# Kernel tuning notes

Hardware: AMD Instinct MI355X
Metric: run time of the kernel (lower is better)

The kernel has to match this reference:

```python
import jax, jax.numpy as jnp
import numpy as np

B, OBS, TASK = 65536, 512, 128
D, M, N = 64, 32, 4  # embedding dim, module width, modules per layer


def setup_inputs() -> dict:
    key = jax.random.key(0)
    ks = jax.random.split(key, 16)

    def w(k, shape):
        fan_in = shape[-2]
        return jax.random.normal(k, shape, jnp.float32) * np.float32(np.sqrt(2.0 / fan_in))

    z = lambda *s: jnp.zeros(s, jnp.float32)
    return dict(
        obs=jax.random.normal(ks[0], (B, OBS), jnp.float32),
        task=jax.random.normal(ks[1], (B, TASK), jnp.float32),
        Ws1=w(ks[2], (OBS, D)), bs1=z(D),
        Ws2=w(ks[3], (D, D)), bs2=z(D),
        Wt=w(ks[4], (TASK, D)), bt=z(D),
        Wa0=w(ks[5], (D, N * N)), ba0=z(N * N),
        Wa1=w(ks[6], (D, N * N)), ba1=z(N * N),
        Wc0=w(ks[7], (N * N, D)), bc0=z(D),
        Wc1=w(ks[8], (2 * N * N, D)), bc1=z(D),
        We0=w(ks[9], (N, D, M)), be0=z(N, M),
        We1=w(ks[10], (N, M, M)), be1=z(N, M),
        We2=w(ks[11], (N, M, M)), be2=z(N, M),
    )


def reference(obs, task, Ws1, bs1, Ws2, bs2, Wt, bt, Wa0, ba0, Wa1, ba1,
              Wc0, bc0, Wc1, bc1, We0, be0, We1, be1, We2, be2):
    relu = jax.nn.relu
    # base encoders
    s = relu(relu(obs @ Ws1 + bs1) @ Ws2 + bs2)          # [B, D]
    t = relu(task @ Wt + bt)                              # [B, D]
    r0 = s * t                                            # first routing inputs [B, D]
    prev = jnp.broadcast_to(s[None], (N,) + s.shape)      # [N, B, D] (state emb fed to all layer-0 modules)

    # routing layer 0 -> 1
    a0 = jax.nn.softmax((r0 @ Wa0 + ba0).reshape(-1, N, N), axis=-1)   # [B, N_next, N_prev]
    m = relu(jnp.einsum('nbi,nio->nbo', prev, We0) + be0[:, None, :])  # [N, B, M] expert outputs
    prev = jnp.einsum('bij,jbd->ibd', a0, m)                           # [N, B, M] attention-combined
    r = relu((a0.reshape(-1, N * N) @ Wc0 + bc0) * r0)                 # updated routing inputs

    # routing layer 1 -> 2
    a1 = jax.nn.softmax((r @ Wa1 + ba1).reshape(-1, N, N), axis=-1)
    m = relu(jnp.einsum('nbi,nio->nbo', prev, We1) + be1[:, None, :])
    prev = jnp.einsum('bij,jbd->ibd', a1, m)
    attn_cat = jnp.concatenate([a0.reshape(-1, N * N), a1.reshape(-1, N * N)], axis=-1)
    r = relu((attn_cat @ Wc1 + bc1) * r0)  # computed as in original (unused afterward)

    # final module layer, plain sum over modules
    m = relu(jnp.einsum('nbi,nio->nbo', prev, We2) + be2[:, None, :])  # [N, B, M]
    return relu(m.sum(axis=0))                                          # [B, M]
```

## Files before the change

### kernel.cpp

```cpp
#include <hip/hip_runtime.h>
#include <hip/hip_bf16.h>


using f32x4 = __attribute__((ext_vector_type(4))) float;
using h16x4 = __attribute__((ext_vector_type(4))) _Float16;

#define MFMA16(a, b, c) __builtin_amdgcn_mfma_f32_16x16x16f16((a), (b), (c), 0, 0, 0)

__device__ __forceinline__ short h_bits(float f) {
  _Float16 h = (_Float16)f;
  return __builtin_bit_cast(short, h);
}

__device__ __forceinline__ void dma16(const void* g, void* l) {
  __builtin_amdgcn_global_load_lds(
      (const __attribute__((address_space(1))) unsigned int*)g,
      (__attribute__((address_space(3))) unsigned int*)l, 16, 0, 0);
}

__global__ void sm_convert_v4(
    const float* __restrict__ Ws1, const float* __restrict__ Ws2, const float* __restrict__ Wt,
    const float* __restrict__ Wa0, const float* __restrict__ Wa1, const float* __restrict__ Wc0,
    const float* __restrict__ We0, const float* __restrict__ We1, const float* __restrict__ We2,
    const float* __restrict__ bs1, const float* __restrict__ bs2, const float* __restrict__ bt,
    const float* __restrict__ ba0, const float* __restrict__ ba1, const float* __restrict__ bc0,
    const float* __restrict__ be0, const float* __restrict__ be1, const float* __restrict__ be2,
    short* __restrict__ wsh, float* __restrict__ biasf) {
  int d = blockIdx.x * 256 + threadIdx.x;
  if (d < 64512) {
    float v;
    if (d < 32768) {
      int kk = d & 3, nt = (d >> 2) & 3, p = (d >> 4) & 15, q = (d >> 8) & 3, c = d >> 10;
      int k = c * 16 + q * 4 + kk, o = nt * 16 + p;
      v = Ws1[k * 64 + o];
    }
    else if (d < 36864) { int r = d - 32768, o = r >> 6, k = r & 63;   v = Ws2[k * 64 + o]; }
    else if (d < 45056) {
      int r = d - 36864;
      int kk = r & 3, nt = (r >> 2) & 3, p = (r >> 4) & 15, q = (r >> 8) & 3, c = r >> 10;
      int k = c * 16 + q * 4 + kk, o = nt * 16 + p;
      v = Wt[k * 64 + o];
    }
    else if (d < 46080) { int r = d - 45056, o = r >> 6, k = r & 63;   v = Wa0[k * 16 + o]; }
    else if (d < 47104) { int r = d - 46080, o = r >> 6, k = r & 63;   v = Wa1[k * 16 + o]; }
    else if (d < 48128) { int r = d - 47104, o = r >> 4, k = r & 15;   v = Wc0[k * 64 + o]; }
    else if (d < 56320) { int r = d - 48128, n = r >> 11, o = (r >> 6) & 31, i = r & 63; v = We0[n * 2048 + i * 32 + o]; }
    else if (d < 60416) { int r = d - 56320, n = r >> 10, o = (r >> 5) & 31, i = r & 31; v = We1[n * 1024 + i * 32 + o]; }
    else                { int r = d - 60416, n = r >> 10, o = (r >> 5) & 31, i = r & 31; v = We2[n * 1024 + i * 32 + o]; }
    wsh[d] = h_bits(v);
  } else if (d < 65184) {
    int r = d - 64512;
    float v;
    if      (r < 64)  v = bs1[r];
    else if (r < 128) v = bs2[r - 64];
    else if (r < 192) v = bt[r - 128];
    else if (r < 208) v = ba0[r - 192];
    else if (r < 224) v = ba1[r - 208];
    else if (r < 288) v = bc0[r - 224];
    else if (r < 416) v = be0[r - 288];
    else if (r < 544) v = be1[r - 416];
    else              v = be2[r - 544];
    biasf[r] = v;
  }
}

__global__ __launch_bounds__(256) void sm_fused_v4(
    const float* __restrict__ obs, const float* __restrict__ task,
    const short* __restrict__ wsh, const float* __restrict__ biasf,
    float* __restrict__ out) {
  const int tid  = threadIdx.x;
  const int wave = tid >> 6;
  const int lane = tid & 63;
  const int q    = lane >> 4;
  const int p    = lane & 15;
  const int lrow = wave * 16;
  const int rowblk = blockIdx.x * 64 + lrow;

  __shared__ __align__(16) char lds[9216 + 3072 + 8192 + 20480];
  char* x_lds = lds;
  char* a_lds = lds + 9216;
  char* ring  = lds + 12288 + wave * 2048;
  char* p_lds = lds + 20480;

  const short* Bp1  = wsh;
  const short* Ws2T = wsh + 32768;
  const short* WtP  = wsh + 36864;
  const short* Wa0T = wsh + 45056;
  const short* Wa1T = wsh + 46080;
  const short* Wc0T = wsh + 47104;
  const short* We0T = wsh + 48128;
  const short* We1T = wsh + 56320;
  const short* We2T = wsh + 60416;
  const float* bs1 = biasf;        const float* bs2 = biasf + 64;
  const float* bt  = biasf + 128;  const float* ba0 = biasf + 192;
  const float* ba1 = biasf + 208;  const float* bc0 = biasf + 224;
  const float* be0 = biasf + 288;  const float* be1 = biasf + 416;
  const float* be2 = biasf + 544;

  const f32x4 z4 = {0.f, 0.f, 0.f, 0.f};

  auto stx  = [&](int row, int col, float v) { *(short*)(x_lds + row * 144 + col * 2) = h_bits(v); };
  auto ldx4 = [&](int row, int k0) -> h16x4 { return *(const h16x4*)(x_lds + row * 144 + k0 * 2); };
  auto ldb  = [&](const short* W, int off) -> h16x4 { return *(const h16x4*)(W + off); };
  auto cvt4 = [&](const float4& v) -> h16x4 {
    h16x4 a;
    a[0] = (_Float16)v.x; a[1] = (_Float16)v.y;
    a[2] = (_Float16)v.z; a[3] = (_Float16)v.w;
    return a;
  };

  f32x4 accX[4] = {z4, z4, z4, z4};
  {
    const float* srow = obs + (size_t)(rowblk + (lane >> 2)) * 512 + (lane & 3) * 4;
    dma16(srow, ring);
    for (int c = 0; c < 32; ++c) {
      if (c + 1 < 32) {
        dma16(srow + (c + 1) * 16, ring + ((c + 1) & 1) * 1024);
        asm volatile("s_waitcnt vmcnt(1)" ::: "memory");
      } else {
        asm volatile("s_waitcnt vmcnt(0)" ::: "memory");
      }
      const char* sb = ring + (c & 1) * 1024;
      h16x4 a = cvt4(*(const float4*)(sb + p * 64 + q * 16));
      const short* bp = Bp1 + ((c * 4 + q) * 16 + p) * 16;
#pragma unroll
      for (int nt = 0; nt < 4; ++nt)
        accX[nt] = MFMA16(a, ldb(bp, nt * 4), accX[nt]);
    }
  }
#pragma unroll
  for (int nt = 0; nt < 4; ++nt) {
    float bias = bs1[nt * 16 + p];
#pragma unroll
    for (int r = 0; r < 4; ++r)
      stx(lrow + 4 * q + r, nt * 16 + p, fmaxf(accX[nt][r] + bias, 0.f));
  }

  f32x4 accS[4] = {z4, z4, z4, z4};
#pragma unroll
  for (int kb = 0; kb < 4; ++kb) {
    h16x4 a = ldx4(lrow + p, kb * 16 + q * 4);
#pragma unroll
    for (int nt = 0; nt < 4; ++nt)
      accS[nt] = MFMA16(a, ldb(Ws2T, (nt * 16 + p) * 64 + kb * 16 + q * 4), accS[nt]);
  }
  float sf[4][4];
#pragma unroll
  for (int nt = 0; nt < 4; ++nt) {
    float bias = bs2[nt * 16 + p];
#pragma unroll
    for (int r = 0; r < 4; ++r) sf[nt][r] = fmaxf(accS[nt][r] + bias, 0.f);
  }
#pragma unroll
  for (int nt = 0; nt < 4; ++nt)
#pragma unroll
    for (int r = 0; r < 4; ++r) stx(lrow + 4 * q + r, nt * 16 + p, sf[nt][r]);

  f32x4 accT[4] = {z4, z4, z4, z4};
  {
    const float* srow = task + (size_t)(rowblk + (lane >> 2)) * 128 + (lane & 3) * 4;
    dma16(srow, ring);
    for (int c = 0; c < 8; ++c) {
      if (c + 1 < 8) {
        dma16(srow + (c + 1) * 16, ring + ((c + 1) & 1) * 1024);
        asm volatile("s_waitcnt vmcnt(1)" ::: "memory");
      } else {
        asm volatile("s_waitcnt vmcnt(0)" ::: "memory");
      }
      const char* sb = ring + (c & 1) * 1024;
      h16x4 a = cvt4(*(const float4*)(sb + p * 64 + q * 16));
      const short* bp = WtP + ((c * 4 + q) * 16 + p) * 16;
#pragma unroll
      for (int nt = 0; nt < 4; ++nt)
        accT[nt] = MFMA16(a, ldb(bp, nt * 4), accT[nt]);
    }
  }
  float r0f[4][4];
#pragma unroll
  for (int nt = 0; nt < 4; ++nt) {
    float bias = bt[nt * 16 + p];
#pragma unroll
    for (int r = 0; r < 4; ++r)
      r0f[nt][r] = sf[nt][r] * fmaxf(accT[nt][r] + bias, 0.f);
  }

  float mfr[4][2][4];
#pragma unroll
  for (int n = 0; n < 4; ++n) {
    f32x4 acc[2] = {z4, z4};
#pragma unroll
    for (int kb = 0; kb < 4; ++kb) {
      h16x4 a = ldx4(lrow + p, kb * 16 + q * 4);
#pragma unroll
      for (int nt = 0; nt < 2; ++nt)
        acc[nt] = MFMA16(a, ldb(We0T, (n * 32 + nt * 16 + p) * 64 + kb * 16 + q * 4), acc[nt]);
    }
#pragma unroll
    for (int nt = 0; nt < 2; ++nt) {
      float bias = be0[n * 32 + nt * 16 + p];
#pragma unroll
      for (int r = 0; r < 4; ++r) mfr[n][nt][r] = fmaxf(acc[nt][r] + bias, 0.f);
    }
  }

#pragma unroll
  for (int nt = 0; nt < 4; ++nt)
#pragma unroll
    for (int r = 0; r < 4; ++r) stx(lrow + 4 * q + r, nt * 16 + p, r0f[nt][r]);

  f32x4 accA = z4;
#pragma unroll
  for (int kb = 0; kb < 4; ++kb)
    accA = MFMA16(ldx4(lrow + p, kb * 16 + q * 4), ldb(Wa0T, p * 64 + kb * 16 + q * 4), accA);
  float a0v[4];
  {
    float bias = ba0[p];
#pragma unroll
    for (int r = 0; r < 4; ++r) {
      float v = accA[r] + bias;
      float mx = fmaxf(v, __shfl_xor(v, 1));
      mx = fmaxf(mx, __shfl_xor(mx, 2));
      float e = __expf(v - mx);
      float ssum = e + __shfl_xor(e, 1);
      ssum += __shfl_xor(ssum, 2);
      a0v[r] = e / ssum;
    }
  }
#pragma unroll
  for (int r = 0; r < 4; ++r)
    *(short*)(a_lds + (lrow + 4 * q + r) * 48 + p * 2) = h_bits(a0v[r]);

  float pv[4][2][4];
#pragma unroll
  for (int i = 0; i < 4; ++i)
#pragma unroll
    for (int nt = 0; nt < 2; ++nt)
#pragma unroll
      for (int r = 0; r < 4; ++r) pv[i][nt][r] = 0.f;
  const int sbase = lane & 48;
#pragma unroll
  for (int r = 0; r < 4; ++r) {
#pragma unroll
    for (int c = 0; c < 16; ++c) {
      float av = __shfl(a0v[r], sbase | c);
      pv[c >> 2][0][r] += av * mfr[c & 3][0][r];
      pv[c >> 2][1][r] += av * mfr[c & 3][1][r];
    }
  }

  f32x4 accC[4] = {z4, z4, z4, z4};
  {
    h16x4 a = *(const h16x4*)(a_lds + (lrow + p) * 48 + q * 8);
#pragma unroll
    for (int nt = 0; nt < 4; ++nt)
      accC[nt] = MFMA16(a, ldb(Wc0T, (nt * 16 + p) * 16 + q * 4), accC[nt]);
  }
  float rf[4][4];
#pragma unroll
  for (int nt = 0; nt < 4; ++nt) {
    float bias = bc0[nt * 16 + p];
#pragma unroll
    for (int r = 0; r < 4; ++r)
      rf[nt][r] = fmaxf((accC[nt][r] + bias) * r0f[nt][r], 0.f);
  }
#pragma unroll
  for (int nt = 0; nt < 4; ++nt)
#pragma unroll
    for (int r = 0; r < 4; ++r) stx(lrow + 4 * q + r, nt * 16 + p, rf[nt][r]);

  f32x4 accA1 = z4;
#pragma unroll
  for (int kb = 0; kb < 4; ++kb)
    accA1 = MFMA16(ldx4(lrow + p, kb * 16 + q * 4), ldb(Wa1T, p * 64 + kb * 16 + q * 4), accA1);
  float a1v[4];
  {
    float bias = ba1[p];
#pragma unroll
    for (int r = 0; r < 4; ++r) {
      float v = accA1[r] + bias;
      float mx = fmaxf(v, __shfl_xor(v, 1));
      mx = fmaxf(mx, __shfl_xor(mx, 2));
      float e = __expf(v - mx);
      float ssum = e + __shfl_xor(e, 1);
      ssum += __shfl_xor(ssum, 2);
      a1v[r] = e / ssum;
    }
  }

#pragma unroll
  for (int i = 0; i < 4; ++i)
#pragma unroll
    for (int nt = 0; nt < 2; ++nt)
#pragma unroll
      for (int r = 0; r < 4; ++r)
        *(short*)(p_lds + (i * 64 + lrow + 4 * q + r) * 80 + (nt * 16 + p) * 2) = h_bits(pv[i][nt][r]);

  float m1f[4][2][4];
#pragma unroll
  for (int n = 0; n < 4; ++n) {
    f32x4 acc[2] = {z4, z4};
#pragma unroll
    for (int kb = 0; kb < 2; ++kb) {
      h16x4 a = *(const h16x4*)(p_lds + (n * 64 + lrow + p) * 80 + kb * 32 + q * 8);
#pragma unroll
      for (int nt = 0; nt < 2; ++nt)
        acc[nt] = MFMA16(a, ldb(We1T, (n * 32 + nt * 16 + p) * 32 + kb * 16 + q * 4), acc[nt]);
    }
#pragma unroll
    for (int nt = 0; nt < 2; ++nt) {
      float bias = be1[n * 32 + nt * 16 + p];
#pragma unroll
      for (int r = 0; r < 4; ++r) m1f[n][nt][r] = fmaxf(acc[nt][r] + bias, 0.f);
    }
  }

#pragma unroll
  for (int i = 0; i < 4; ++i)
#pragma unroll
    for (int nt = 0; nt < 2; ++nt)
#pragma unroll
      for (int r = 0; r < 4; ++r) pv[i][nt][r] = 0.f;
#pragma unroll
  for (int r = 0; r < 4; ++r) {
#pragma unroll
    for (int c = 0; c < 16; ++c) {
      float av = __shfl(a1v[r], sbase | c);
      pv[c >> 2][0][r] += av * m1f[c & 3][0][r];
      pv[c >> 2][1][r] += av * m1f[c & 3][1][r];
    }
  }

#pragma unroll
  for (int i = 0; i < 4; ++i)
#pragma unroll
    for (int nt = 0; nt < 2; ++nt)
#pragma unroll
      for (int r = 0; r < 4; ++r)
        *(short*)(p_lds + (i * 64 + lrow + 4 * q + r) * 80 + (nt * 16 + p) * 2) = h_bits(pv[i][nt][r]);

  float of[2][4] = {{0.f, 0.f, 0.f, 0.f}, {0.f, 0.f, 0.f, 0.f}};
#pragma unroll
  for (int n = 0; n < 4; ++n) {
    f32x4 acc[2] = {z4, z4};
#pragma unroll
    for (int kb = 0; kb < 2; ++kb) {
      h16x4 a = *(const h16x4*)(p_lds + (n * 64 + lrow + p) * 80 + kb * 32 + q * 8);
#pragma unroll
      for (int nt = 0; nt < 2; ++nt)
        acc[nt] = MFMA16(a, ldb(We2T, (n * 32 + nt * 16 + p) * 32 + kb * 16 + q * 4), acc[nt]);
    }
#pragma unroll
    for (int nt = 0; nt < 2; ++nt) {
      float bias = be2[n * 32 + nt * 16 + p];
#pragma unroll
      for (int r = 0; r < 4; ++r) of[nt][r] += fmaxf(acc[nt][r] + bias, 0.f);
    }
  }
#pragma unroll
  for (int nt = 0; nt < 2; ++nt)
#pragma unroll
    for (int r = 0; r < 4; ++r) {
      int grow = rowblk + 4 * q + r;
      out[(size_t)grow * 32 + nt * 16 + p] = of[nt][r];
    }
}

extern "C" void kernel_launch(void* const* d_in, const int* in_sizes, int n_in,
                              void* d_out, int out_size, void* d_ws, size_t ws_size,
                              hipStream_t stream) {
  (void)in_sizes; (void)n_in; (void)out_size; (void)ws_size;
  const float* obs  = (const float*)d_in[0];
  const float* task = (const float*)d_in[1];
  const float* Ws1 = (const float*)d_in[2];  const float* bs1 = (const float*)d_in[3];
  const float* Ws2 = (const float*)d_in[4];  const float* bs2 = (const float*)d_in[5];
  const float* Wt  = (const float*)d_in[6];  const float* bt  = (const float*)d_in[7];
  const float* Wa0 = (const float*)d_in[8];  const float* ba0 = (const float*)d_in[9];
  const float* Wa1 = (const float*)d_in[10]; const float* ba1 = (const float*)d_in[11];
  const float* Wc0 = (const float*)d_in[12]; const float* bc0 = (const float*)d_in[13];
  const float* We0 = (const float*)d_in[16]; const float* be0 = (const float*)d_in[17];
  const float* We1 = (const float*)d_in[18]; const float* be1 = (const float*)d_in[19];
  const float* We2 = (const float*)d_in[20]; const float* be2 = (const float*)d_in[21];

  short* wsh   = (short*)d_ws;
  float* biasf = (float*)((char*)d_ws + 129040);

  sm_convert_v4<<<dim3(255), dim3(256), 0, stream>>>(
      Ws1, Ws2, Wt, Wa0, Wa1, Wc0, We0, We1, We2,
      bs1, bs2, bt, ba0, ba1, bc0, be0, be1, be2,
      wsh, biasf);
  sm_fused_v4<<<dim3(1024), dim3(256), 0, stream>>>(
      obs, task, wsh, biasf, (float*)d_out);
}
```

Baseline: 82.62 us.

## Replace LDS DMA ring with register-prefetched direct loads and alias LDS buffers

The obs and task GEMM input streams no longer go through a global_load_lds double-buffered ring. They now load directly into registers with a three-deep prefetch, fetching A fragments and B weight fragments as 16-byte vectors. The per-chunk waitcnt stalls and the LDS round trip are dropped. The p_lds buffer is aliased onto the x_lds/a_lds region behind a new __syncthreads, cutting LDS from about 40KB to 20KB so more blocks can be resident. The cost is higher register pressure from the prefetch buffers, plus one block-wide barrier.

```diff
diff --git a/kernel.cpp b/kernel.cpp
--- a/kernel.cpp
+++ b/kernel.cpp
@@ -4,6 +4,8 @@
 
 using f32x4 = __attribute__((ext_vector_type(4))) float;
 using h16x4 = __attribute__((ext_vector_type(4))) _Float16;
+using u32x4 = __attribute__((ext_vector_type(4))) unsigned int;
+using u32x2 = __attribute__((ext_vector_type(2))) unsigned int;
 
 #define MFMA16(a, b, c) __builtin_amdgcn_mfma_f32_16x16x16f16((a), (b), (c), 0, 0, 0)
 
@@ -12,13 +14,7 @@
   return __builtin_bit_cast(short, h);
 }
 
-__device__ __forceinline__ void dma16(const void* g, void* l) {
-  __builtin_amdgcn_global_load_lds(
-      (const __attribute__((address_space(1))) unsigned int*)g,
-      (__attribute__((address_space(3))) unsigned int*)l, 16, 0, 0);
-}
-
-__global__ void sm_convert_v4(
+__global__ void sm_convert_v6(
     const float* __restrict__ Ws1, const float* __restrict__ Ws2, const float* __restrict__ Wt,
     const float* __restrict__ Wa0, const float* __restrict__ Wa1, const float* __restrict__ Wc0,
     const float* __restrict__ We0, const float* __restrict__ We1, const float* __restrict__ We2,
@@ -64,7 +60,7 @@
   }
 }
 
-__global__ __launch_bounds__(256) void sm_fused_v4(
+__global__ __launch_bounds__(256) void sm_fused_v6(
     const float* __restrict__ obs, const float* __restrict__ task,
     const short* __restrict__ wsh, const float* __restrict__ biasf,
     float* __restrict__ out) {
@@ -76,11 +72,10 @@
   const int lrow = wave * 16;
   const int rowblk = blockIdx.x * 64 + lrow;
 
-  __shared__ __align__(16) char lds[9216 + 3072 + 8192 + 20480];
+  __shared__ __align__(16) char lds[20480];
   char* x_lds = lds;
   char* a_lds = lds + 9216;
-  char* ring  = lds + 12288 + wave * 2048;
-  char* p_lds = lds + 20480;
+  char* p_lds = lds;
 
   const short* Bp1  = wsh;
   const short* Ws2T = wsh + 32768;
@@ -102,30 +97,41 @@
   auto stx  = [&](int row, int col, float v) { *(short*)(x_lds + row * 144 + col * 2) = h_bits(v); };
   auto ldx4 = [&](int row, int k0) -> h16x4 { return *(const h16x4*)(x_lds + row * 144 + k0 * 2); };
   auto ldb  = [&](const short* W, int off) -> h16x4 { return *(const h16x4*)(W + off); };
-  auto cvt4 = [&](const float4& v) -> h16x4 {
+  auto cvtA = [&](const u32x4& u) -> h16x4 {
+    float4 v = __builtin_bit_cast(float4, u);
     h16x4 a;
     a[0] = (_Float16)v.x; a[1] = (_Float16)v.y;
     a[2] = (_Float16)v.z; a[3] = (_Float16)v.w;
     return a;
   };
+  auto lo2 = [&](const u32x4& u) -> h16x4 { return __builtin_bit_cast(h16x4, (u32x2){u[0], u[1]}); };
+  auto hi2 = [&](const u32x4& u) -> h16x4 { return __builtin_bit_cast(h16x4, (u32x2){u[2], u[3]}); };
 
   f32x4 accX[4] = {z4, z4, z4, z4};
   {
-    const float* srow = obs + (size_t)(rowblk + (lane >> 2)) * 512 + (lane & 3) * 4;
-    dma16(srow, ring);
+    const float* aptr = obs + (size_t)(rowblk + p) * 512 + q * 4;
+    u32x4 Ab[3], B0[3], B1[3];
+#pragma unroll
+    for (int i = 0; i < 3; ++i) {
+      Ab[i] = *(const u32x4*)(aptr + i * 16);
+      const short* bp = Bp1 + ((i * 4 + q) * 16 + p) * 16;
+      B0[i] = *(const u32x4*)bp;
+      B1[i] = *(const u32x4*)(bp + 8);
+    }
+#pragma unroll
     for (int c = 0; c < 32; ++c) {
-      if (c + 1 < 32) {
-        dma16(srow + (c + 1) * 16, ring + ((c + 1) & 1) * 1024);
-        asm volatile("s_waitcnt vmcnt(1)" ::: "memory");
-      } else {
-        asm volatile("s_waitcnt vmcnt(0)" ::: "memory");
+      const int s = c % 3;
+      h16x4 a = cvtA(Ab[s]);
+      accX[0] = MFMA16(a, lo2(B0[s]), accX[0]);
+      accX[1] = MFMA16(a, hi2(B0[s]), accX[1]);
+      accX[2] = MFMA16(a, lo2(B1[s]), accX[2]);
+      accX[3] = MFMA16(a, hi2(B1[s]), accX[3]);
+      if (c + 3 < 32) {
+        Ab[s] = *(const u32x4*)(aptr + (c + 3) * 16);
+        const short* bp = Bp1 + (((c + 3) * 4 + q) * 16 + p) * 16;
+        B0[s] = *(const u32x4*)bp;
+        B1[s] = *(const u32x4*)(bp + 8);
       }
-      const char* sb = ring + (c & 1) * 1024;
-      h16x4 a = cvt4(*(const float4*)(sb + p * 64 + q * 16));
-      const short* bp = Bp1 + ((c * 4 + q) * 16 + p) * 16;
-#pragma unroll
-      for (int nt = 0; nt < 4; ++nt)
-        accX[nt] = MFMA16(a, ldb(bp, nt * 4), accX[nt]);
     }
   }
 #pragma unroll
@@ -158,21 +164,29 @@
 
   f32x4 accT[4] = {z4, z4, z4, z4};
   {
-    const float* srow = task + (size_t)(rowblk + (lane >> 2)) * 128 + (lane & 3) * 4;
-    dma16(srow, ring);
+    const float* aptr = task + (size_t)(rowblk + p) * 128 + q * 4;
+    u32x4 Ab[3], B0[3], B1[3];
+#pragma unroll
+    for (int i = 0; i < 3; ++i) {
+      Ab[i] = *(const u32x4*)(aptr + i * 16);
+      const short* bp = WtP + ((i * 4 + q) * 16 + p) * 16;
+      B0[i] = *(const u32x4*)bp;
+      B1[i] = *(const u32x4*)(bp + 8);
+    }
+#pragma unroll
     for (int c = 0; c < 8; ++c) {
-      if (c + 1 < 8) {
-        dma16(srow + (c + 1) * 16, ring + ((c + 1) & 1) * 1024);
-        asm volatile("s_waitcnt vmcnt(1)" ::: "memory");
-      } else {
-        asm volatile("s_waitcnt vmcnt(0)" ::: "memory");
+      const int s = c % 3;
+      h16x4 a = cvtA(Ab[s]);
+      accT[0] = MFMA16(a, lo2(B0[s]), accT[0]);
+      accT[1] = MFMA16(a, hi2(B0[s]), accT[1]);
+      accT[2] = MFMA16(a, lo2(B1[s]), accT[2]);
+      accT[3] = MFMA16(a, hi2(B1[s]), accT[3]);
+      if (c + 3 < 8) {
+        Ab[s] = *(const u32x4*)(aptr + (c + 3) * 16);
+        const short* bp = WtP + (((c + 3) * 4 + q) * 16 + p) * 16;
+        B0[s] = *(const u32x4*)bp;
+        B1[s] = *(const u32x4*)(bp + 8);
       }
-      const char* sb = ring + (c & 1) * 1024;
-      h16x4 a = cvt4(*(const float4*)(sb + p * 64 + q * 16));
-      const short* bp = WtP + ((c * 4 + q) * 16 + p) * 16;
-#pragma unroll
-      for (int nt = 0; nt < 4; ++nt)
-        accT[nt] = MFMA16(a, ldb(bp, nt * 4), accT[nt]);
     }
   }
   float r0f[4][4];
@@ -286,6 +300,8 @@
       a1v[r] = e / ssum;
     }
   }
+
+  __syncthreads();
 
 #pragma unroll
   for (int i = 0; i < 4; ++i)
@@ -384,10 +400,10 @@
   short* wsh   = (short*)d_ws;
   float* biasf = (float*)((char*)d_ws + 129040);
 
-  sm_convert_v4<<<dim3(255), dim3(256), 0, stream>>>(
+  sm_convert_v6<<<dim3(255), dim3(256), 0, stream>>>(
       Ws1, Ws2, Wt, Wa0, Wa1, Wc0, We0, We1, We2,
       bs1, bs2, bt, ba0, ba1, bc0, be0, be1, be2,
       wsh, biasf);
-  sm_fused_v4<<<dim3(1024), dim3(256), 0, stream>>>(
+  sm_fused_v6<<<dim3(1024), dim3(256), 0, stream>>>(
       obs, task, wsh, biasf, (float*)d_out);
 }
```

New measurement: 98.26 us. 18.9% more time.

## Stage obs/task tiles block-wide with XOR-swizzled 32-column LDS chunks

Applied to the files above, without the earlier changes.

Input staging changes from per-wave 16-float chunks to cooperative block-wide DMA of 32-column tiles (8 KB per buffer, double-buffered) into a shared ring. An XOR swizzle on the 16-byte column index avoids LDS bank conflicts, and weight B fragments are fetched as 16-byte vectors. The task tile's first stage is issued early so it overlaps the Ws2 layer, and p_lds now aliases x_lds to shrink LDS. This halves the outer loop trip count and makes each global request larger, at the cost of two __syncthreads per chunk and an extra barrier before p_lds is reused.

```diff
diff --git a/kernel.cpp b/kernel.cpp
--- a/kernel.cpp
+++ b/kernel.cpp
@@ -4,6 +4,8 @@
 
 using f32x4 = __attribute__((ext_vector_type(4))) float;
 using h16x4 = __attribute__((ext_vector_type(4))) _Float16;
+using u32x4 = __attribute__((ext_vector_type(4))) unsigned int;
+using u32x2 = __attribute__((ext_vector_type(2))) unsigned int;
 
 #define MFMA16(a, b, c) __builtin_amdgcn_mfma_f32_16x16x16f16((a), (b), (c), 0, 0, 0)
 
@@ -12,13 +14,13 @@
   return __builtin_bit_cast(short, h);
 }
 
-__device__ __forceinline__ void dma16(const void* g, void* l) {
+__device__ __forceinline__ void dma16(const float* g, char* l) {
   __builtin_amdgcn_global_load_lds(
       (const __attribute__((address_space(1))) unsigned int*)g,
       (__attribute__((address_space(3))) unsigned int*)l, 16, 0, 0);
 }
 
-__global__ void sm_convert_v4(
+__global__ void sm_convert_v7(
     const float* __restrict__ Ws1, const float* __restrict__ Ws2, const float* __restrict__ Wt,
     const float* __restrict__ Wa0, const float* __restrict__ Wa1, const float* __restrict__ Wc0,
     const float* __restrict__ We0, const float* __restrict__ We1, const float* __restrict__ We2,
@@ -30,15 +32,15 @@
   if (d < 64512) {
     float v;
     if (d < 32768) {
-      int kk = d & 3, nt = (d >> 2) & 3, p = (d >> 4) & 15, q = (d >> 8) & 3, c = d >> 10;
-      int k = c * 16 + q * 4 + kk, o = nt * 16 + p;
+      int kk = d & 3, nt = (d >> 2) & 3, p = (d >> 4) & 15, q = (d >> 8) & 3, cc = d >> 10;
+      int k = cc * 16 + q * 4 + kk, o = nt * 16 + p;
       v = Ws1[k * 64 + o];
     }
     else if (d < 36864) { int r = d - 32768, o = r >> 6, k = r & 63;   v = Ws2[k * 64 + o]; }
     else if (d < 45056) {
       int r = d - 36864;
-      int kk = r & 3, nt = (r >> 2) & 3, p = (r >> 4) & 15, q = (r >> 8) & 3, c = r >> 10;
-      int k = c * 16 + q * 4 + kk, o = nt * 16 + p;
+      int kk = r & 3, nt = (r >> 2) & 3, p = (r >> 4) & 15, q = (r >> 8) & 3, cc = r >> 10;
+      int k = cc * 16 + q * 4 + kk, o = nt * 16 + p;
       v = Wt[k * 64 + o];
     }
     else if (d < 46080) { int r = d - 45056, o = r >> 6, k = r & 63;   v = Wa0[k * 16 + o]; }
@@ -64,7 +66,7 @@
   }
 }
 
-__global__ __launch_bounds__(256) void sm_fused_v4(
+__global__ __launch_bounds__(256) void sm_fused_v7(
     const float* __restrict__ obs, const float* __restrict__ task,
     const short* __restrict__ wsh, const float* __restrict__ biasf,
     float* __restrict__ out) {
@@ -74,13 +76,14 @@
   const int q    = lane >> 4;
   const int p    = lane & 15;
   const int lrow = wave * 16;
-  const int rowblk = blockIdx.x * 64 + lrow;
-
-  __shared__ __align__(16) char lds[9216 + 3072 + 8192 + 20480];
+  const int wgrow  = blockIdx.x * 64;
+  const int rowblk = wgrow + lrow;
+
+  __shared__ __align__(16) char lds[28672];
   char* x_lds = lds;
   char* a_lds = lds + 9216;
-  char* ring  = lds + 12288 + wave * 2048;
-  char* p_lds = lds + 20480;
+  char* ring  = lds + 12288;
+  char* p_lds = lds;
 
   const short* Bp1  = wsh;
   const short* Ws2T = wsh + 32768;
@@ -102,30 +105,55 @@
   auto stx  = [&](int row, int col, float v) { *(short*)(x_lds + row * 144 + col * 2) = h_bits(v); };
   auto ldx4 = [&](int row, int k0) -> h16x4 { return *(const h16x4*)(x_lds + row * 144 + k0 * 2); };
   auto ldb  = [&](const short* W, int off) -> h16x4 { return *(const h16x4*)(W + off); };
-  auto cvt4 = [&](const float4& v) -> h16x4 {
+  auto cvtA = [&](const u32x4& u) -> h16x4 {
+    float4 v = __builtin_bit_cast(float4, u);
     h16x4 a;
     a[0] = (_Float16)v.x; a[1] = (_Float16)v.y;
     a[2] = (_Float16)v.z; a[3] = (_Float16)v.w;
     return a;
   };
+  auto lo2 = [&](const u32x4& u) -> h16x4 { return __builtin_bit_cast(h16x4, (u32x2){u[0], u[1]}); };
+  auto hi2 = [&](const u32x4& u) -> h16x4 { return __builtin_bit_cast(h16x4, (u32x2){u[2], u[3]}); };
+
+  auto stage = [&](const float* base, int rowlen, int k0, int buf) {
+#pragma unroll
+    for (int j = 0; j < 2; ++j) {
+      int f = j * 256 + wave * 64 + lane;
+      int row = f >> 3;
+      int cl = (f & 7) ^ (row & 7);
+      const float* g = base + (size_t)(wgrow + row) * rowlen + k0 + cl * 4;
+      dma16(g, ring + buf * 8192 + (j * 256 + wave * 64) * 16);
+    }
+  };
+  auto lda = [&](int buf, int kb2) -> u32x4 {
+    return *(const u32x4*)(ring + buf * 8192 + (lrow + p) * 128 +
+                           (((kb2 * 4 + q) ^ (p & 7)) * 16));
+  };
 
   f32x4 accX[4] = {z4, z4, z4, z4};
   {
-    const float* srow = obs + (size_t)(rowblk + (lane >> 2)) * 512 + (lane & 3) * 4;
-    dma16(srow, ring);
-    for (int c = 0; c < 32; ++c) {
-      if (c + 1 < 32) {
-        dma16(srow + (c + 1) * 16, ring + ((c + 1) & 1) * 1024);
-        asm volatile("s_waitcnt vmcnt(1)" ::: "memory");
+    stage(obs, 512, 0, 0);
+    for (int c = 0; c < 16; ++c) {
+      if (c + 1 < 16) {
+        stage(obs, 512, (c + 1) * 32, (c + 1) & 1);
+        asm volatile("s_waitcnt vmcnt(2)" ::: "memory");
       } else {
         asm volatile("s_waitcnt vmcnt(0)" ::: "memory");
       }
-      const char* sb = ring + (c & 1) * 1024;
-      h16x4 a = cvt4(*(const float4*)(sb + p * 64 + q * 16));
-      const short* bp = Bp1 + ((c * 4 + q) * 16 + p) * 16;
-#pragma unroll
-      for (int nt = 0; nt < 4; ++nt)
-        accX[nt] = MFMA16(a, ldb(bp, nt * 4), accX[nt]);
+      __syncthreads();
+#pragma unroll
+      for (int kb2 = 0; kb2 < 2; ++kb2) {
+        const int cc = c * 2 + kb2;
+        const short* bp = Bp1 + ((cc * 4 + q) * 16 + p) * 16;
+        u32x4 B0 = *(const u32x4*)bp;
+        u32x4 B1 = *(const u32x4*)(bp + 8);
+        h16x4 a = cvtA(lda(c & 1, kb2));
+        accX[0] = MFMA16(a, lo2(B0), accX[0]);
+        accX[1] = MFMA16(a, hi2(B0), accX[1]);
+        accX[2] = MFMA16(a, lo2(B1), accX[2]);
+        accX[3] = MFMA16(a, hi2(B1), accX[3]);
+      }
+      __syncthreads();
     }
   }
 #pragma unroll
@@ -136,6 +164,8 @@
       stx(lrow + 4 * q + r, nt * 16 + p, fmaxf(accX[nt][r] + bias, 0.f));
   }
 
+  stage(task, 128, 0, 0);
+
   f32x4 accS[4] = {z4, z4, z4, z4};
 #pragma unroll
   for (int kb = 0; kb < 4; ++kb) {
@@ -158,21 +188,27 @@
 
   f32x4 accT[4] = {z4, z4, z4, z4};
   {
-    const float* srow = task + (size_t)(rowblk + (lane >> 2)) * 128 + (lane & 3) * 4;
-    dma16(srow, ring);
-    for (int c = 0; c < 8; ++c) {
-      if (c + 1 < 8) {
-        dma16(srow + (c + 1) * 16, ring + ((c + 1) & 1) * 1024);
-        asm volatile("s_waitcnt vmcnt(1)" ::: "memory");
+    for (int c = 0; c < 4; ++c) {
+      if (c + 1 < 4) {
+        stage(task, 128, (c + 1) * 32, (c + 1) & 1);
+        asm volatile("s_waitcnt vmcnt(2)" ::: "memory");
       } else {
         asm volatile("s_waitcnt vmcnt(0)" ::: "memory");
       }
-      const char* sb = ring + (c & 1) * 1024;
-      h16x4 a = cvt4(*(const float4*)(sb + p * 64 + q * 16));
-      const short* bp = WtP + ((c * 4 + q) * 16 + p) * 16;
-#pragma unroll
-      for (int nt = 0; nt < 4; ++nt)
-        accT[nt] = MFMA16(a, ldb(bp, nt * 4), accT[nt]);
+      __syncthreads();
+#pragma unroll
+      for (int kb2 = 0; kb2 < 2; ++kb2) {
+        const int cc = c * 2 + kb2;
+        const short* bp = WtP + ((cc * 4 + q) * 16 + p) * 16;
+        u32x4 B0 = *(const u32x4*)bp;
+        u32x4 B1 = *(const u32x4*)(bp + 8);
+        h16x4 a = cvtA(lda(c & 1, kb2));
+        accT[0] = MFMA16(a, lo2(B0), accT[0]);
+        accT[1] = MFMA16(a, hi2(B0), accT[1]);
+        accT[2] = MFMA16(a, lo2(B1), accT[2]);
+        accT[3] = MFMA16(a, hi2(B1), accT[3]);
+      }
+      __syncthreads();
     }
   }
   float r0f[4][4];
@@ -286,6 +322,8 @@
       a1v[r] = e / ssum;
     }
   }
+
+  __syncthreads();
 
 #pragma unroll
   for (int i = 0; i < 4; ++i)
@@ -384,10 +422,10 @@
   short* wsh   = (short*)d_ws;
   float* biasf = (float*)((char*)d_ws + 129040);
 
-  sm_convert_v4<<<dim3(255), dim3(256), 0, stream>>>(
+  sm_convert_v7<<<dim3(255), dim3(256), 0, stream>>>(
       Ws1, Ws2, Wt, Wa0, Wa1, Wc0, We0, We1, We2,
       bs1, bs2, bt, ba0, ba1, bc0, be0, be1, be2,
       wsh, biasf);
-  sm_fused_v4<<<dim3(1024), dim3(256), 0, stream>>>(
+  sm_fused_v7<<<dim3(1024), dim3(256), 0, stream>>>(
       obs, task, wsh, biasf, (float*)d_out);
 }
```

Measured after the change: 79.67 us. 1.04x faster.
